# Optimization experiments

Measured on AMD Instinct MI355X. Metric: run time of the kernel, lower is better.

The kernel has to match this reference:

```python
import jax, jax.numpy as jnp
import numpy as np

B, N, K, CIN, COUT, H = 4, 2048, 32, 16, 32, 32
EPS = 1e-5


def setup_inputs() -> dict:
    key = jax.random.key(0)
    ks = jax.random.split(key, 6)
    s = 0.1
    return dict(
        xyz=jax.random.uniform(ks[0], (B, N, 3), dtype=jnp.float32),
        points=jax.random.normal(ks[1], (B, N, CIN), dtype=jnp.float32),
        W1=jax.random.normal(ks[2], (3, H), dtype=jnp.float32) * s,
        b1=jnp.zeros((H,), jnp.float32),
        g1=jnp.ones((H,), jnp.float32),
        be1=jnp.zeros((H,), jnp.float32),
        W2=jax.random.normal(ks[3], (H, H), dtype=jnp.float32) * s,
        b2=jnp.zeros((H,), jnp.float32),
        g2=jnp.ones((H,), jnp.float32),
        be2=jnp.zeros((H,), jnp.float32),
        W3=jax.random.normal(ks[4], (H, CIN * COUT), dtype=jnp.float32) * s,
        b3=jnp.zeros((CIN * COUT,), jnp.float32),
        gbn=jnp.ones((COUT,), jnp.float32),
        bbn=jnp.zeros((COUT,), jnp.float32),
    )


def _bn(h, g, b):
    # BatchNorm1d training-mode math: biased batch stats over axis 0
    return g * (h - h.mean(0)) / jnp.sqrt(h.var(0) + EPS) + b


def reference(xyz, points, W1, b1, g1, be1, W2, b2, g2, be2, W3, b3, gbn, bbn):
    # KNN: squared distances (B,N,N)
    sq = jnp.sum(xyz * xyz, -1)
    dist = -2.0 * jnp.einsum('bmc,bnc->bmn', xyz, xyz) + sq[:, :, None] + sq[:, None, :]
    _, idx = jax.lax.top_k(-dist, K)  # (B,N,K) nearest neighbors

    gather = jax.vmap(lambda p, i: p[i])  # (N,C),(N,K)->(N,K,C), vmapped over B
    grouped_xyz = gather(xyz, idx)                      # (B,N,K,3)
    rel = grouped_xyz - xyz[:, :, None, :]              # (B,N,K,3)
    grouped_pts = gather(points, idx)                   # (B,N,K,CIN)

    # weight net on relative coords
    h = rel.reshape(-1, 3)
    h = _bn(jax.nn.relu(h @ W1 + b1), g1, be1)
    h = _bn(jax.nn.relu(h @ W2 + b2), g2, be2)
    w = (h @ W3 + b3).reshape(B, N, K, CIN, COUT)       # (B,N,K,CIN,COUT)

    # weighted sum over C_in, then max over neighbors
    out = jnp.einsum('bnkc,bnkco->bnko', grouped_pts, w)  # (B,N,K,COUT)
    out = out.max(axis=2)                                 # (B,N,COUT)

    # final BatchNorm1d over (B,N) per channel
    m = out.mean((0, 1))
    v = out.var((0, 1))
    return gbn * (out - m) / jnp.sqrt(v + EPS) + bbn
```

## Files before the change

kernel.cpp:

```cpp
#include <hip/hip_runtime.h>

#define B_ 4
#define N_ 2048
#define K_ 32
#define CIN_ 16
#define COUT_ 32
#define H_ 32
#define R_ (B_*N_*K_)
#define EPS_ 1e-5f
#define INVR_ (1.0f/(float)R_)
#define INVBN_ (1.0f/(float)(B_*N_))
#define LISTCAP 160
#define NSH 16

typedef __attribute__((ext_vector_type(8)))  _Float16 f16x8;
typedef __attribute__((ext_vector_type(2)))  __fp16   hw16x2;
typedef __attribute__((ext_vector_type(2)))  _Float16 f16x2;
typedef __attribute__((ext_vector_type(16))) float    f32x16;

__device__ __forceinline__ float dot3f(float ax,float ay,float az,float bx,float by,float bz){
    return fmaf(az,bz, fmaf(ay,by, ax*bx));
}
__device__ __forceinline__ unsigned int pk2(float a, float b){
    union { hw16x2 v; unsigned int u; } c;
    c.v = __builtin_amdgcn_cvt_pkrtz(a, b);
    return c.u;
}
__device__ __forceinline__ unsigned int pkmul(unsigned int a, unsigned int b){
    union { unsigned int u; f16x2 v; } x, y, r;
    x.u = a; y.u = b; r.v = x.v * y.v; return r.u;
}
__device__ __forceinline__ float shsum(const float* __restrict__ p, int k){
    float s = 0.f;
    #pragma unroll
    for (int i = 0; i < NSH; ++i) s += p[i*32 + k];
    return s;
}

__global__ __launch_bounds__(256) void k_prep0(const float* __restrict__ xyz, const float* __restrict__ points,
                                               float4* __restrict__ xs4g, unsigned int* __restrict__ pf16,
                                               float* __restrict__ st){
    int flat = blockIdx.x*256 + threadIdx.x;
    if (flat < 8192){
        float x = xyz[3*flat], y = xyz[3*flat+1], z = xyz[3*flat+2];
        xs4g[flat] = make_float4(x, y, z, dot3f(x,y,z,x,y,z));
    } else {
        int p = flat - 8192;
        pf16[p] = pk2(points[2*p], points[2*p+1]);
    }
    if (blockIdx.x == 0){
        for (int j = threadIdx.x; j < 1280; j += 256) st[j] = 0.f;
    }
}

__global__ __launch_bounds__(256,7) void k_knn(const float4* __restrict__ xs4g,
                                               const float* __restrict__ W1, const float* __restrict__ b1,
                                               int* __restrict__ idx_out,
                                               float* __restrict__ s1sh, float* __restrict__ q1sh,
                                               unsigned int* __restrict__ h1f){
    __shared__ unsigned int hist[4][512][2];
    __shared__ unsigned long long lst[4][LISTCAP];
    __shared__ int kidx[4][K_];

    const int tid  = threadIdx.x;
    const int w    = tid >> 6;
    const int lane = tid & 63;
    const int half = lane >> 5;
    const int b    = blockIdx.x >> 9;
    const int q    = ((blockIdx.x & 511) << 2) + w;
    const int bN   = b * N_;
    unsigned int* hw = &hist[w][0][0];

    const uint4 z4 = make_uint4(0,0,0,0);
    uint4* h4 = (uint4*)hw;
    #pragma unroll
    for (int i = 0; i < 4; ++i) h4[i*64 + lane] = z4;

    const float4 qp = xs4g[bN + q];
    const float qx = qp.x, qy = qp.y, qz = qp.z, sqq = qp.w;

    unsigned int fv[32];
    #pragma unroll
    for (int j = 0; j < 32; ++j){
        int c = j*64 + lane;
        float4 pt = xs4g[bN + c];
        float d = fmaf(-2.0f, dot3f(qx,qy,qz, pt.x,pt.y,pt.z), sqq) + pt.w;
        fv[j] = __float_as_uint(d);
        unsigned int u1 = __float_as_uint(d + 1.0f);
        unsigned int key = (u1 <= 0x3F800000u) ? 0u : ((u1 - 0x3F800000u) >> 15);
        key = key > 511u ? 511u : key;
        atomicAdd(&hw[key*2 + (lane & 1)], 1u);
    }

    unsigned int g[8];
    #pragma unroll
    for (int t = 0; t < 4; ++t){
        uint4 h = ((const uint4*)hw)[lane*4 + t];
        g[2*t]   = h.x + h.y;
        g[2*t+1] = h.z + h.w;
    }
    unsigned int gs = 0;
    #pragma unroll
    for (int t = 0; t < 8; ++t) gs += g[t];
    unsigned int cum = gs;
    #pragma unroll
    for (int off = 1; off < 64; off <<= 1){
        unsigned int v = __shfl_up(cum, off);
        if (lane >= off) cum += v;
    }
    unsigned long long bal = __ballot(cum >= (unsigned)K_);
    int L = __ffsll(bal) - 1;
    unsigned int run = __shfl(cum, L) - __shfl(gs, L);
    int Bsel = 8*L + 7;
    {
        unsigned int c = run; bool fnd = false;
        #pragma unroll
        for (int t = 0; t < 8; ++t){
            unsigned int ht = __shfl(g[t], L, 64);
            if (!fnd && c + ht >= (unsigned)K_){ Bsel = 8*L + t; fnd = true; }
            c += ht;
        }
    }
    const float Tedge = __uint_as_float(0x3F800000u + ((unsigned)(Bsel + 1) << 15));
    const bool allin = (Bsel == 511);

    const unsigned long long mlt = (lane == 63) ? ~0ull >> 1 : (1ull << lane) - 1ull;
    unsigned int cnt = 0;
    #pragma unroll
    for (int j = 0; j < 32; ++j){
        float f1 = __uint_as_float(fv[j]) + 1.0f;
        bool surv = (f1 < Tedge) || allin;
        unsigned long long sb = __ballot(surv);
        unsigned int pos = cnt + (unsigned int)__popcll(sb & mlt);
        if (surv && pos < (unsigned)LISTCAP)
            lst[w][pos] = ((unsigned long long)fv[j] << 32) | (unsigned int)(j*64 + lane);
        cnt += (unsigned int)__popcll(sb);
    }
    int m = (int)cnt; if (m > LISTCAP) m = LISTCAP;

    int* outp = idx_out + ((size_t)bN + q) * K_;
    for (int i = lane; i < m; i += 64){
        unsigned long long my = lst[w][i];
        int rank = 0;
        for (int jj = 0; jj < m; ++jj)
            rank += (lst[w][jj] < my) ? 1 : 0;
        if (rank < K_){
            int id = (int)(unsigned int)(my & 0xFFFFFFFFull);
            outp[rank] = id;
            kidx[w][rank] = id;
        }
    }

    {
        const int ch = lane & 31;
        float w1a = W1[ch], w1b = W1[H_+ch], w1c = W1[2*H_+ch], b1c = b1[ch];
        float s = 0.f, qq = 0.f;
        #pragma unroll
        for (int r = 0; r < 16; ++r){
            int idr = kidx[w][half*16 + r];
            float4 pn = xs4g[bN + idr];
            float rx = pn.x - qx, ry = pn.y - qy, rz = pn.z - qz;
            float h = fmaxf(fmaf(rx, w1a, fmaf(ry, w1b, fmaf(rz, w1c, b1c))), 0.0f);
            s += h; qq = fmaf(h, h, qq);
        }
        s  += __shfl_xor(s, 32, 64);
        qq += __shfl_xor(qq, 32, 64);
        if (lane < 32){
            int sh = (blockIdx.x & (NSH-1)) * 32 + ch;
            atomicAdd(&s1sh[sh], s);
            atomicAdd(&q1sh[sh], qq);
        }
    }

    {
        const int id = kidx[w][lane & 31];
        float4 pn = xs4g[bN + id];
        float rx = pn.x - qx, ry = pn.y - qy, rz = pn.z - qz;
        uint4* dst = (uint4*)h1f + (size_t)(bN + q)*128 + lane;
        const int c0 = half*8;
        #pragma unroll
        for (int sblk = 0; sblk < 2; ++sblk){
            const int cb = sblk*16 + c0;
            const float4 wa0 = *(const float4*)(W1 + cb);
            const float4 wa1 = *(const float4*)(W1 + cb + 4);
            const float4 wb0 = *(const float4*)(W1 + H_ + cb);
            const float4 wb1 = *(const float4*)(W1 + H_ + cb + 4);
            const float4 wc0 = *(const float4*)(W1 + 2*H_ + cb);
            const float4 wc1 = *(const float4*)(W1 + 2*H_ + cb + 4);
            const float4 bv0 = *(const float4*)(b1 + cb);
            const float4 bv1 = *(const float4*)(b1 + cb + 4);
            float h0 = fmaxf(fmaf(rx, wa0.x, fmaf(ry, wb0.x, fmaf(rz, wc0.x, bv0.x))), 0.0f);
            float h1v= fmaxf(fmaf(rx, wa0.y, fmaf(ry, wb0.y, fmaf(rz, wc0.y, bv0.y))), 0.0f);
            float h2v= fmaxf(fmaf(rx, wa0.z, fmaf(ry, wb0.z, fmaf(rz, wc0.z, bv0.z))), 0.0f);
            float h3 = fmaxf(fmaf(rx, wa0.w, fmaf(ry, wb0.w, fmaf(rz, wc0.w, bv0.w))), 0.0f);
            float h4 = fmaxf(fmaf(rx, wa1.x, fmaf(ry, wb1.x, fmaf(rz, wc1.x, bv1.x))), 0.0f);
            float h5 = fmaxf(fmaf(rx, wa1.y, fmaf(ry, wb1.y, fmaf(rz, wc1.y, bv1.y))), 0.0f);
            float h6 = fmaxf(fmaf(rx, wa1.z, fmaf(ry, wb1.z, fmaf(rz, wc1.z, bv1.z))), 0.0f);
            float h7 = fmaxf(fmaf(rx, wa1.w, fmaf(ry, wb1.w, fmaf(rz, wc1.w, bv1.w))), 0.0f);
            uint4 o;
            o.x = pk2(h0, h1v); o.y = pk2(h2v, h3); o.z = pk2(h4, h5); o.w = pk2(h6, h7);
            dst[sblk*64] = o;
        }
    }
}

__global__ __launch_bounds__(256) void k_prep2(const float* __restrict__ s1s, const float* __restrict__ q1s,
                                               const float* __restrict__ g1, const float* __restrict__ be1,
                                               const float* __restrict__ W2, const float* __restrict__ b2,
                                               unsigned int* __restrict__ W2f, float* __restrict__ b2p){
    int flat = blockIdx.x*256 + threadIdx.x;
    if (flat < 512){
        int d = flat;
        int jj = d & 3, lane = (d >> 2) & 63, s = d >> 8;
        int col = lane & 31;
        int k0 = s*16 + (lane >> 5)*8 + 2*jj;
        float m0 = shsum(s1s,k0)*INVR_,   v0 = shsum(q1s,k0)*INVR_   - m0*m0;
        float m1 = shsum(s1s,k0+1)*INVR_, v1 = shsum(q1s,k0+1)*INVR_ - m1*m1;
        float a0  = g1[k0]   / sqrtf(v0 + EPS_);
        float a1v = g1[k0+1] / sqrtf(v1 + EPS_);
        W2f[d] = pk2(a0*W2[k0*H_ + col], a1v*W2[(k0+1)*H_ + col]);
    } else if (flat < 544){
        int col = flat - 512;
        float acc = b2[col];
        #pragma unroll 4
        for (int h = 0; h < H_; ++h){
            float mm = shsum(s1s,h)*INVR_, vv = shsum(q1s,h)*INVR_ - mm*mm;
            float aa = g1[h] / sqrtf(vv + EPS_);
            float bb = fmaf(-aa, mm, be1[h]);
            acc = fmaf(bb, W2[h*H_ + col], acc);
        }
        b2p[col] = acc;
    }
}

__global__ __launch_bounds__(256,4) void k_h2stats(const uint4* __restrict__ h1f,
                                                   const uint4* __restrict__ W2f, const float* __restrict__ b2p,
                                                   float* gsum, float* gsq){
    __shared__ float redS[H_], redQ[H_];
    const int tid = threadIdx.x, lane = tid & 63, w = tid >> 6;
    const int m = lane & 31;
    if (tid < H_){ redS[tid] = 0.f; redQ[tid] = 0.f; }
    __syncthreads();

    union { uint4 u4; f16x8 v; } Bf0, Bf1;
    Bf0.u4 = W2f[lane];
    Bf1.u4 = W2f[64 + lane];
    float b2c = b2p[m];
    const int blk0 = blockIdx.x*8 + w*2;

    float s = 0.f, q = 0.f;
    #pragma unroll
    for (int t = 0; t < 2; ++t){
        union { uint4 u4; f16x8 v; } a0, a1f;
        a0.u4  = h1f[(size_t)(blk0 + t)*128 + lane];
        a1f.u4 = h1f[(size_t)(blk0 + t)*128 + 64 + lane];
        f32x16 acc;
        #pragma unroll
        for (int i = 0; i < 16; ++i) acc[i] = b2c;
        acc = __builtin_amdgcn_mfma_f32_32x32x16_f16(a0.v,  Bf0.v, acc, 0, 0, 0);
        acc = __builtin_amdgcn_mfma_f32_32x32x16_f16(a1f.v, Bf1.v, acc, 0, 0, 0);
        #pragma unroll
        for (int i = 0; i < 16; ++i){
            float v = fmaxf(acc[i], 0.0f);
            s += v; q = fmaf(v, v, q);
        }
    }
    s += __shfl_xor(s, 32, 64);
    q += __shfl_xor(q, 32, 64);
    if (lane < 32){ atomicAdd(&redS[m], s); atomicAdd(&redQ[m], q); }
    __syncthreads();
    if (tid < H_){ atomicAdd(&gsum[tid], redS[tid]); atomicAdd(&gsq[tid], redQ[tid]); }
}

__global__ __launch_bounds__(256) void k_prep3(const float* __restrict__ W3, const float* __restrict__ b3,
                                               const float* __restrict__ s2, const float* __restrict__ q2,
                                               const float* __restrict__ g2, const float* __restrict__ be2,
                                               unsigned int* __restrict__ W3f){
    int d = blockIdx.x*256 + threadIdx.x;
    int jj = d & 3, lane = (d >> 2) & 63, step = d >> 8;
    int col = lane & 31;
    int off = (lane >> 5)*8 + 2*jj;
    float v0, v1;
    if (step < 32){
        int h = step, c0 = off;
        float mm = s2[h]*INVR_, vv = q2[h]*INVR_ - mm*mm;
        float aa = g2[h] / sqrtf(vv + EPS_);
        v0 = aa * W3[h*512 + c0*COUT_ + col];
        v1 = aa * W3[h*512 + (c0+1)*COUT_ + col];
    } else {
        int c0 = off;
        v0 = b3[c0*COUT_ + col]; v1 = b3[(c0+1)*COUT_ + col];
        #pragma unroll 4
        for (int h = 0; h < H_; ++h){
            float mm = s2[h]*INVR_, vv = q2[h]*INVR_ - mm*mm;
            float aa = g2[h] / sqrtf(vv + EPS_);
            float bb = fmaf(-aa, mm, be2[h]);
            v0 = fmaf(bb, W3[h*512 + c0*COUT_ + col], v0);
            v1 = fmaf(bb, W3[h*512 + (c0+1)*COUT_ + col], v1);
        }
    }
    W3f[d] = pk2(v0, v1);
}

#define PHASEA(T, H2P, GSEL) do { \
    union { uint4 u4; f16x8 v; } B0f, B1f; \
    B0f.u4 = h1f[(size_t)(blk0 + (T))*128 + lane]; \
    B1f.u4 = h1f[(size_t)(blk0 + (T))*128 + 64 + lane]; \
    int row = rB + (T)*32 + m; \
    int bb_ = row >> 16; \
    int idr = idx[row]; \
    const uint4* gpp = (const uint4*)(pf16 + ((size_t)bb_*N_ + idr)*8); \
    uint4 ga = gpp[0], gb = gpp[1]; \
    GSEL[0] = half ? gb.x : ga.x; \
    GSEL[1] = half ? gb.y : ga.y; \
    GSEL[2] = half ? gb.z : ga.z; \
    GSEL[3] = half ? gb.w : ga.w; \
    f32x16 c2; \
    _Pragma("unroll") \
    for (int i = 0; i < 16; ++i) c2[i] = b2v[i]; \
    c2 = __builtin_amdgcn_mfma_f32_32x32x16_f16(A0.v, B0f.v, c2, 0, 0, 0); \
    c2 = __builtin_amdgcn_mfma_f32_32x32x16_f16(A1.v, B1f.v, c2, 0, 0, 0); \
    _Pragma("unroll") \
    for (int p = 0; p < 8; ++p){ \
        float v0 = fmaxf(c2[2*p],   0.0f); \
        float v1 = fmaxf(c2[2*p+1], 0.0f); \
        unsigned int ow = pk2(v0, v1); \
        unsigned int ot = __shfl_xor(ow, 32, 64); \
        int a = p >> 1, bb = p & 1; \
        H2P[4*a + bb]     = half ? ot : ow; \
        H2P[4*a + 2 + bb] = half ? ow : ot; \
    } \
} while(0)

#define REDST(ACC, T) do { \
    float v = ACC[0]; \
    _Pragma("unroll") \
    for (int i = 1; i < 16; ++i) v = fmaxf(v, ACC[i]); \
    v = fmaxf(v, __shfl_xor(v, 32, 64)); \
    if (lane < 32){ \
        int g = blk0 + (T); \
        out_pre[(size_t)g*COUT_ + m] = v; \
        atomicAdd(&redS[m], v); \
        atomicAdd(&redQ[m], v*v); \
    } \
} while(0)

__global__ __launch_bounds__(256,4) void k_out(const uint4* __restrict__ h1f, const int* __restrict__ idx,
                                               const uint4* __restrict__ W2f, const float* __restrict__ b2p,
                                               const unsigned int* __restrict__ pf16,
                                               const uint4* __restrict__ W3f,
                                               float* __restrict__ out_pre, float* gsum, float* gsq){
    __shared__ uint4 Wls[2112];
    __shared__ float redS[COUT_], redQ[COUT_];
    const int tid = threadIdx.x, lane = tid & 63, w = tid >> 6;
    const int half = lane >> 5, m = lane & 31;
    for (int i = tid; i < 2112; i += 256) Wls[i] = W3f[i];
    if (tid < COUT_){ redS[tid] = 0.f; redQ[tid] = 0.f; }
    __syncthreads();

    const int rB = blockIdx.x*256 + w*64;
    const int blk0 = blockIdx.x*8 + w*2;

    union { uint4 u4; f16x8 v; } A0, A1;
    A0.u4 = W2f[lane];
    A1.u4 = W2f[64 + lane];
    float b2v[16];
    #pragma unroll
    for (int i = 0; i < 16; ++i) b2v[i] = b2p[(i&3) + 8*(i>>2) + 4*half];

    unsigned int h2p0[16], h2p1[16];
    unsigned int gsel0[4], gsel1[4];
    PHASEA(0, h2p0, gsel0);
    PHASEA(1, h2p1, gsel1);

    f32x16 acc0, acc1;
    #pragma unroll
    for (int i = 0; i < 16; ++i){ acc0[i] = 0.f; acc1[i] = 0.f; }
    #pragma unroll
    for (int kb = 0; kb < 32; ++kb){
        union { uint4 u4; f16x8 v; } bf; bf.u4 = Wls[kb*64 + lane];
        const unsigned int sel = (kb & 1) ? 0x03020302u : 0x01000100u;
        unsigned int hr0 = h2p0[kb >> 1];
        unsigned int hd0 = __builtin_amdgcn_perm(hr0, hr0, sel);
        union { unsigned int u[4]; f16x8 v; } af;
        #pragma unroll
        for (int jj = 0; jj < 4; ++jj) af.u[jj] = pkmul(hd0, gsel0[jj]);
        acc0 = __builtin_amdgcn_mfma_f32_32x32x16_f16(af.v, bf.v, acc0, 0, 0, 0);
        unsigned int hr1 = h2p1[kb >> 1];
        unsigned int hd1 = __builtin_amdgcn_perm(hr1, hr1, sel);
        #pragma unroll
        for (int jj = 0; jj < 4; ++jj) af.u[jj] = pkmul(hd1, gsel1[jj]);
        acc1 = __builtin_amdgcn_mfma_f32_32x32x16_f16(af.v, bf.v, acc1, 0, 0, 0);
    }
    {
        union { uint4 u4; f16x8 v; } bf; bf.u4 = Wls[32*64 + lane];
        union { unsigned int u[4]; f16x8 v; } af;
        #pragma unroll
        for (int jj = 0; jj < 4; ++jj) af.u[jj] = gsel0[jj];
        acc0 = __builtin_amdgcn_mfma_f32_32x32x16_f16(af.v, bf.v, acc0, 0, 0, 0);
        #pragma unroll
        for (int jj = 0; jj < 4; ++jj) af.u[jj] = gsel1[jj];
        acc1 = __builtin_amdgcn_mfma_f32_32x32x16_f16(af.v, bf.v, acc1, 0, 0, 0);
    }

    REDST(acc0, 0);
    REDST(acc1, 1);

    __syncthreads();
    if (tid < COUT_){ atomicAdd(&gsum[tid], redS[tid]); atomicAdd(&gsq[tid], redQ[tid]); }
}

__global__ __launch_bounds__(256) void k_bn(const float* __restrict__ out_pre,
                                            const float* __restrict__ s3, const float* __restrict__ q3,
                                            const float* __restrict__ gbn, const float* __restrict__ bbn,
                                            float* __restrict__ out){
    int i = blockIdx.x*256 + threadIdx.x;
    int o = i & (COUT_-1);
    float mm = s3[o] * INVBN_;
    float vv = q3[o] * INVBN_ - mm*mm;
    float aa = gbn[o] / sqrtf(vv + EPS_);
    out[i] = fmaf(aa, out_pre[i], fmaf(-aa, mm, bbn[o]));
}

extern "C" void kernel_launch(void* const* d_in, const int* in_sizes, int n_in,
                              void* d_out, int out_size, void* d_ws, size_t ws_size,
                              hipStream_t stream){
    const float* xyz    = (const float*)d_in[0];
    const float* points = (const float*)d_in[1];
    const float* W1  = (const float*)d_in[2];
    const float* b1  = (const float*)d_in[3];
    const float* g1  = (const float*)d_in[4];
    const float* be1 = (const float*)d_in[5];
    const float* W2  = (const float*)d_in[6];
    const float* b2  = (const float*)d_in[7];
    const float* g2  = (const float*)d_in[8];
    const float* be2 = (const float*)d_in[9];
    const float* W3  = (const float*)d_in[10];
    const float* b3  = (const float*)d_in[11];
    const float* gbn = (const float*)d_in[12];
    const float* bbn = (const float*)d_in[13];
    float* out = (float*)d_out;

    char* base = (char*)d_ws;
    int*            idx     = (int*)(base + 0);
    float*          out_pre = (float*)(base + 1048576);
    unsigned int*   pf16    = (unsigned int*)(base + 2097152);
    unsigned int*   W3f     = (unsigned int*)(base + 2359296);
    unsigned int*   W2f     = (unsigned int*)(base + 2393088);
    float*          b2p     = (float*)(base + 2395136);
    float*          st      = (float*)(base + 2395264);
    float4*         xs4g    = (float4*)(base + 2400384);
    unsigned int*   h1f     = (unsigned int*)(base + 4194304);
    float *s1s=st, *q1s=st+512, *s2=st+1024, *q2=st+1056, *s3=st+1088, *q3=st+1120;

    hipLaunchKernelGGL(k_prep0,   dim3(288),      dim3(256), 0, stream, xyz, points, xs4g, pf16, st);
    hipLaunchKernelGGL(k_knn,     dim3(B_*N_/4),  dim3(256), 0, stream, xs4g, W1, b1, idx, s1s, q1s, h1f);
    hipLaunchKernelGGL(k_prep2,   dim3(3),        dim3(256), 0, stream, s1s, q1s, g1, be1, W2, b2, W2f, b2p);
    hipLaunchKernelGGL(k_h2stats, dim3(R_/256),   dim3(256), 0, stream, (const uint4*)h1f,
                       (const uint4*)W2f, b2p, s2, q2);
    hipLaunchKernelGGL(k_prep3,   dim3(33),       dim3(256), 0, stream, W3, b3, s2, q2, g2, be2, W3f);
    hipLaunchKernelGGL(k_out,     dim3(R_/256),   dim3(256), 0, stream, (const uint4*)h1f, idx,
                       (const uint4*)W2f, b2p, pf16, (const uint4*)W3f, out_pre, s3, q3);
    hipLaunchKernelGGL(k_bn,      dim3(B_*N_*COUT_/256), dim3(256), 0, stream, out_pre, s3, q3, gbn, bbn, out);
}
```

Before: 176.0 us.

## Recompute KNN distances instead of caching, double h2stats work per block, vectorize BN

The KNN kernel stops holding 32 per-lane distances in registers and recomputes them in the compaction pass from xs4g, with partial unrolling. The aim is lower register pressure and higher occupancy, at the cost of a second read of the point coordinates. k_h2stats now has each wave process four row tiles instead of two, which halves the grid and the number of per-block atomic flushes. The final BN kernel is vectorized to float4 loads and stores over a quarter of the threads.

```diff
diff --git a/kernel.cpp b/kernel.cpp
--- a/kernel.cpp
+++ b/kernel.cpp
@@ -79,13 +79,11 @@
     const float4 qp = xs4g[bN + q];
     const float qx = qp.x, qy = qp.y, qz = qp.z, sqq = qp.w;
 
-    unsigned int fv[32];
-    #pragma unroll
+    #pragma unroll 4
     for (int j = 0; j < 32; ++j){
         int c = j*64 + lane;
         float4 pt = xs4g[bN + c];
         float d = fmaf(-2.0f, dot3f(qx,qy,qz, pt.x,pt.y,pt.z), sqq) + pt.w;
-        fv[j] = __float_as_uint(d);
         unsigned int u1 = __float_as_uint(d + 1.0f);
         unsigned int key = (u1 <= 0x3F800000u) ? 0u : ((u1 - 0x3F800000u) >> 15);
         key = key > 511u ? 511u : key;
@@ -126,14 +124,17 @@
 
     const unsigned long long mlt = (lane == 63) ? ~0ull >> 1 : (1ull << lane) - 1ull;
     unsigned int cnt = 0;
-    #pragma unroll
+    #pragma unroll 4
     for (int j = 0; j < 32; ++j){
-        float f1 = __uint_as_float(fv[j]) + 1.0f;
+        int c = j*64 + lane;
+        float4 pt = xs4g[bN + c];
+        float d = fmaf(-2.0f, dot3f(qx,qy,qz, pt.x,pt.y,pt.z), sqq) + pt.w;
+        float f1 = d + 1.0f;
         bool surv = (f1 < Tedge) || allin;
         unsigned long long sb = __ballot(surv);
         unsigned int pos = cnt + (unsigned int)__popcll(sb & mlt);
         if (surv && pos < (unsigned)LISTCAP)
-            lst[w][pos] = ((unsigned long long)fv[j] << 32) | (unsigned int)(j*64 + lane);
+            lst[w][pos] = ((unsigned long long)__float_as_uint(d) << 32) | (unsigned int)c;
         cnt += (unsigned int)__popcll(sb);
     }
     int m = (int)cnt; if (m > LISTCAP) m = LISTCAP;
@@ -246,11 +247,11 @@
     Bf0.u4 = W2f[lane];
     Bf1.u4 = W2f[64 + lane];
     float b2c = b2p[m];
-    const int blk0 = blockIdx.x*8 + w*2;
+    const int blk0 = blockIdx.x*16 + w*4;
 
     float s = 0.f, q = 0.f;
     #pragma unroll
-    for (int t = 0; t < 2; ++t){
+    for (int t = 0; t < 4; ++t){
         union { uint4 u4; f16x8 v; } a0, a1f;
         a0.u4  = h1f[(size_t)(blk0 + t)*128 + lane];
         a1f.u4 = h1f[(size_t)(blk0 + t)*128 + 64 + lane];
@@ -410,16 +411,31 @@
     if (tid < COUT_){ atomicAdd(&gsum[tid], redS[tid]); atomicAdd(&gsq[tid], redQ[tid]); }
 }
 
-__global__ __launch_bounds__(256) void k_bn(const float* __restrict__ out_pre,
+__global__ __launch_bounds__(256) void k_bn(const float4* __restrict__ out_pre4,
                                             const float* __restrict__ s3, const float* __restrict__ q3,
                                             const float* __restrict__ gbn, const float* __restrict__ bbn,
-                                            float* __restrict__ out){
+                                            float4* __restrict__ out4){
     int i = blockIdx.x*256 + threadIdx.x;
-    int o = i & (COUT_-1);
-    float mm = s3[o] * INVBN_;
-    float vv = q3[o] * INVBN_ - mm*mm;
-    float aa = gbn[o] / sqrtf(vv + EPS_);
-    out[i] = fmaf(aa, out_pre[i], fmaf(-aa, mm, bbn[o]));
+    int o = (i*4) & (COUT_-1);
+    float4 v = out_pre4[i];
+    float4 r;
+    {
+        float mm = s3[o]*INVBN_;   float vv = q3[o]*INVBN_   - mm*mm;
+        float aa = gbn[o]/sqrtf(vv+EPS_);   r.x = fmaf(aa, v.x, fmaf(-aa, mm, bbn[o]));
+    }
+    {
+        float mm = s3[o+1]*INVBN_; float vv = q3[o+1]*INVBN_ - mm*mm;
+        float aa = gbn[o+1]/sqrtf(vv+EPS_); r.y = fmaf(aa, v.y, fmaf(-aa, mm, bbn[o+1]));
+    }
+    {
+        float mm = s3[o+2]*INVBN_; float vv = q3[o+2]*INVBN_ - mm*mm;
+        float aa = gbn[o+2]/sqrtf(vv+EPS_); r.z = fmaf(aa, v.z, fmaf(-aa, mm, bbn[o+2]));
+    }
+    {
+        float mm = s3[o+3]*INVBN_; float vv = q3[o+3]*INVBN_ - mm*mm;
+        float aa = gbn[o+3]/sqrtf(vv+EPS_); r.w = fmaf(aa, v.w, fmaf(-aa, mm, bbn[o+3]));
+    }
+    out4[i] = r;
 }
 
 extern "C" void kernel_launch(void* const* d_in, const int* in_sizes, int n_in,
@@ -456,10 +472,11 @@
     hipLaunchKernelGGL(k_prep0,   dim3(288),      dim3(256), 0, stream, xyz, points, xs4g, pf16, st);
     hipLaunchKernelGGL(k_knn,     dim3(B_*N_/4),  dim3(256), 0, stream, xs4g, W1, b1, idx, s1s, q1s, h1f);
     hipLaunchKernelGGL(k_prep2,   dim3(3),        dim3(256), 0, stream, s1s, q1s, g1, be1, W2, b2, W2f, b2p);
-    hipLaunchKernelGGL(k_h2stats, dim3(R_/256),   dim3(256), 0, stream, (const uint4*)h1f,
+    hipLaunchKernelGGL(k_h2stats, dim3(R_/512),   dim3(256), 0, stream, (const uint4*)h1f,
                        (const uint4*)W2f, b2p, s2, q2);
     hipLaunchKernelGGL(k_prep3,   dim3(33),       dim3(256), 0, stream, W3, b3, s2, q2, g2, be2, W3f);
     hipLaunchKernelGGL(k_out,     dim3(R_/256),   dim3(256), 0, stream, (const uint4*)h1f, idx,
                        (const uint4*)W2f, b2p, pf16, (const uint4*)W3f, out_pre, s3, q3);
-    hipLaunchKernelGGL(k_bn,      dim3(B_*N_*COUT_/256), dim3(256), 0, stream, out_pre, s3, q3, gbn, bbn, out);
-}
+    hipLaunchKernelGGL(k_bn,      dim3(256),      dim3(256), 0, stream, (const float4*)out_pre, s3, q3,
+                       gbn, bbn, (float4*)out);
+}
```

New measurement: 178.7 us. No clear change (+1.5%).
